# Kernel tuning notes

Hardware: AMD Instinct MI355X
Metric: run time of the kernel (lower is better)

Reference implementation:

```python
import jax, jax.numpy as jnp
import numpy as np
import math

LAMBDA_ATTRACT = 2.5
REPEL_STRENGTH = 0.15
EPSILON = 0.1  # repulsion distance offset
NORM_EPS = 1e-8
TAU_WEIGHT = 0.3
N = 8192


def _pairwise_angular(theta):
    # angular_distance(theta_i, theta_j) = min(|a-b|, 2*pi - |a-b|), shape [n, n]
    diff = jnp.abs(theta[:, None] - theta[None, :])
    return jnp.minimum(diff, 2.0 * math.pi - diff)


def setup_inputs() -> dict:
    key = jax.random.key(0)
    k1, k2 = jax.random.split(key)
    theta = jax.random.uniform(k1, (N,), dtype=jnp.float32, minval=-math.pi, maxval=math.pi)
    tau = jax.random.normal(k2, (N,), dtype=jnp.float32)
    return {"theta": theta, "tau": tau}


def reference(theta, tau):
    n = theta.shape[0]
    eye = jnp.eye(n, dtype=bool)

    d_theta = _pairwise_angular(theta)                      # [n, n]
    d_tau = jnp.abs(tau[:, None] - tau[None, :])            # [n, n]
    dist = d_theta + TAU_WEIGHT * d_tau

    # attention: exp(-lambda * dist), diagonal excluded, row-normalized
    dist_no_self = jnp.where(eye, jnp.inf, dist)
    scores = jnp.exp(-LAMBDA_ATTRACT * dist_no_self)
    attn = scores / jnp.sum(scores, axis=1, keepdims=True)

    cos_part = jnp.cos(theta)
    sin_part = jnp.sin(theta)
    R_x = attn @ cos_part
    R_y = attn @ sin_part

    # vectorized O(n^2) repulsion (replaces the python double loop)
    d = d_theta + EPSILON
    strength = REPEL_STRENGTH / (d * d)                     # [n, n]
    dx = cos_part[:, None] - cos_part[None, :]
    dy = sin_part[:, None] - sin_part[None, :]
    norm = jnp.sqrt(dx * dx + dy * dy) + NORM_EPS
    inv = jnp.where(eye, 0.0, strength / norm)              # mask i == j
    repel_force_x = jnp.sum(inv * dx, axis=1)
    repel_force_y = jnp.sum(inv * dy, axis=1)

    force_x = R_x + repel_force_x
    force_y = R_y + repel_force_y
    theta_out = jnp.arctan2(force_y, force_x)
    tau_out = attn @ tau
    return (theta_out, tau_out, attn)
```

## Files before the change

kernel.cpp:

```cpp
#include <hip/hip_runtime.h>
#include <math.h>

#define N_PTS 8192
#define TPB 256
#define RPB 8

#define C_LAMBDA   2.5f
#define C_REPEL    0.15f
#define C_EPS      0.1f
#define C_NORM_EPS 1e-8f
#define C_TAUW     0.3f
#define C_TWO_PI   6.28318530717958647692f
#define C_NEG_L_LOG2E (-3.60673760222240625f)

typedef float vf4 __attribute__((ext_vector_type(4)));

__device__ __forceinline__ float fast_exp2(float x) {
#if __has_builtin(__builtin_amdgcn_exp2f)
    return __builtin_amdgcn_exp2f(x);
#else
    return exp2f(x);
#endif
}
__device__ __forceinline__ float fast_sqrt(float x) {
#if __has_builtin(__builtin_amdgcn_sqrtf)
    return __builtin_amdgcn_sqrtf(x);
#else
    return sqrtf(x);
#endif
}
__device__ __forceinline__ float fast_rcp(float x) {
#if __has_builtin(__builtin_amdgcn_rcpf)
    return __builtin_amdgcn_rcpf(x);
#else
    return __fdividef(1.0f, x);
#endif
}
__device__ __forceinline__ float fast_log2(float x) {
#if __has_builtin(__builtin_amdgcn_logf)
    return __builtin_amdgcn_logf(x);
#else
    return log2f(x);
#endif
}

__device__ __forceinline__ float wave_reduce_sum(float v) {
    #pragma unroll
    for (int off = 32; off > 0; off >>= 1)
        v += __shfl_down(v, off, 64);
    return v;
}

__global__ void pack_kernel(const float* __restrict__ theta,
                            const float* __restrict__ tau,
                            float4* __restrict__ pk,
                            float2* __restrict__ pk2) {
    int i = blockIdx.x * blockDim.x + threadIdx.x;
    float t = theta[i];
    float u = tau[i];
    pk[i]  = make_float4(t, u, cosf(t), sinf(t));
    pk2[i] = make_float2(t, u);
}

__global__ __launch_bounds__(TPB) void phase1_kernel(
    const float4* __restrict__ pk,
    float* __restrict__ out,
    float* __restrict__ invsum)
{
    const int tid  = threadIdx.x;
    const int row0 = blockIdx.x * RPB;

    float th_i[RPB], ta_i[RPB], c_i[RPB], s_i[RPB];
    #pragma unroll
    for (int r = 0; r < RPB; ++r) {
        float4 p = pk[row0 + r];
        th_i[r] = p.x; ta_i[r] = p.y; c_i[r] = p.z; s_i[r] = p.w;
    }

    float a_sum[RPB], a_x[RPB], a_y[RPB], a_t[RPB], rp_x[RPB], rp_y[RPB];
    #pragma unroll
    for (int r = 0; r < RPB; ++r) {
        a_sum[r] = 0.f; a_x[r] = 0.f; a_y[r] = 0.f;
        a_t[r] = 0.f; rp_x[r] = 0.f; rp_y[r] = 0.f;
    }

    float4 cur = pk[tid];
    #pragma unroll 2
    for (int k = 0; k < N_PTS / TPB; ++k) {
        float4 nxt = pk[(tid + (k + 1) * TPB) & (N_PTS - 1)];
        #pragma unroll
        for (int r = 0; r < RPB; ++r) {
            float ad    = fabsf(th_i[r] - cur.x);
            float dth   = fminf(ad, C_TWO_PI - ad);
            float t     = fmaf(fabsf(ta_i[r] - cur.y), C_TAUW, dth);
            float score = fast_exp2(t * C_NEG_L_LOG2E);
            a_sum[r] += score;
            a_x[r]   = fmaf(score, cur.z, a_x[r]);
            a_y[r]   = fmaf(score, cur.w, a_y[r]);
            a_t[r]   = fmaf(score, cur.y, a_t[r]);

            float d   = dth + C_EPS;
            float dx  = c_i[r] - cur.z;
            float dy  = s_i[r] - cur.w;
            float q   = fmaf(dx, dx, dy * dy);
            float nrm = fast_sqrt(q) + C_NORM_EPS;
            float inv = fast_rcp(d * d * nrm);
            rp_x[r] = fmaf(inv, dx, rp_x[r]);
            rp_y[r] = fmaf(inv, dy, rp_y[r]);
        }
        cur = nxt;
    }

    __shared__ float red[RPB][6][TPB / 64];
    const int wave = tid >> 6;
    const int lane = tid & 63;
    #pragma unroll
    for (int r = 0; r < RPB; ++r) {
        float v0 = wave_reduce_sum(a_sum[r]);
        float v1 = wave_reduce_sum(a_x[r]);
        float v2 = wave_reduce_sum(a_y[r]);
        float v3 = wave_reduce_sum(a_t[r]);
        float v4 = wave_reduce_sum(rp_x[r]);
        float v5 = wave_reduce_sum(rp_y[r]);
        if (lane == 0) {
            red[r][0][wave] = v0; red[r][1][wave] = v1; red[r][2][wave] = v2;
            red[r][3][wave] = v3; red[r][4][wave] = v4; red[r][5][wave] = v5;
        }
    }
    __syncthreads();

    if (tid < RPB) {
        const int r = tid;
        float s = 0.f, x = 0.f, y = 0.f, t = 0.f, rx = 0.f, ry = 0.f;
        #pragma unroll
        for (int w = 0; w < TPB / 64; ++w) {
            s  += red[r][0][w]; x  += red[r][1][w]; y  += red[r][2][w];
            t  += red[r][3][w]; rx += red[r][4][w]; ry += red[r][5][w];
        }
        float4 p = pk[row0 + r];
        s -= 1.0f;
        x -= p.z;
        y -= p.w;
        t -= p.y;
        float invr = 1.0f / s;
        float fx = fmaf(x, invr, C_REPEL * rx);
        float fy = fmaf(y, invr, C_REPEL * ry);
        out[row0 + r]         = atan2f(fy, fx);
        out[N_PTS + row0 + r] = t * invr;
        invsum[row0 + r]      = invr;
    }
}

__global__ __launch_bounds__(TPB) void phase2_kernel(
    const float2* __restrict__ pk2,
    const float* __restrict__ invsum,
    float* __restrict__ attn)
{
    const int i   = blockIdx.x;
    const int tid = threadIdx.x;
    float2 pi   = pk2[i];
    float th_i  = pi.x;
    float ta_i  = pi.y;
    float l2inv = fast_log2(invsum[i]);
    float* __restrict__ row = attn + (size_t)i * N_PTS;
    const float4* __restrict__ pq = (const float4*)pk2;

    #pragma unroll
    for (int k = 0; k < N_PTS / (TPB * 4); ++k) {
        const int base = tid + k * TPB;
        float4 f1 = pq[2 * base];
        float4 f2 = pq[2 * base + 1];
        const int j0 = 4 * base;

        float ad0  = fabsf(th_i - f1.x);
        float dth0 = fminf(ad0, C_TWO_PI - ad0);
        float t0   = fmaf(fabsf(ta_i - f1.y), C_TAUW, dth0);
        float v0   = fast_exp2(fmaf(t0, C_NEG_L_LOG2E, l2inv));

        float ad1  = fabsf(th_i - f1.z);
        float dth1 = fminf(ad1, C_TWO_PI - ad1);
        float t1   = fmaf(fabsf(ta_i - f1.w), C_TAUW, dth1);
        float v1   = fast_exp2(fmaf(t1, C_NEG_L_LOG2E, l2inv));

        float ad2  = fabsf(th_i - f2.x);
        float dth2 = fminf(ad2, C_TWO_PI - ad2);
        float t2   = fmaf(fabsf(ta_i - f2.y), C_TAUW, dth2);
        float v2   = fast_exp2(fmaf(t2, C_NEG_L_LOG2E, l2inv));

        float ad3  = fabsf(th_i - f2.z);
        float dth3 = fminf(ad3, C_TWO_PI - ad3);
        float t3   = fmaf(fabsf(ta_i - f2.w), C_TAUW, dth3);
        float v3   = fast_exp2(fmaf(t3, C_NEG_L_LOG2E, l2inv));

        vf4 o = {v0, v1, v2, v3};
        __builtin_nontemporal_store(o, (vf4*)(row + j0));
    }

    __syncthreads();
    if (tid == 0) row[i] = 0.0f;
}

extern "C" void kernel_launch(void* const* d_in, const int* in_sizes, int n_in,
                              void* d_out, int out_size, void* d_ws, size_t ws_size,
                              hipStream_t stream) {
    const float* theta = (const float*)d_in[0];
    const float* tau   = (const float*)d_in[1];

    float4* pk     = (float4*)d_ws;
    float2* pk2    = (float2*)((char*)d_ws + 128 * 1024);
    float*  invsum = (float*)((char*)d_ws + 192 * 1024);
    float*  out    = (float*)d_out;
    float*  attn   = out + 2 * N_PTS;

    pack_kernel<<<N_PTS / 256, 256, 0, stream>>>(theta, tau, pk, pk2);
    phase1_kernel<<<N_PTS / RPB, TPB, 0, stream>>>(pk, out, invsum);
    phase2_kernel<<<N_PTS, TPB, 0, stream>>>(pk2, invsum, attn);
}
```

Baseline: 318.3 us.

## Fuse reduction and attention-write kernels into one per-row-block kernel

Merges the phase1 reduction kernel and the phase2 attention-matrix writer into a single kernel. Each block computes its row sums, shares the log2 inverse sums through LDS, then writes those rows of the attention matrix. This removes a launch and the invsum round trip, and lets the long write phase of some blocks overlap with the compute phase of others. RPB drops from 8 to 4 to give more blocks, and the nontemporal stores become plain stores, which may change cache behaviour on the 256MB output write.

Result: faster. 280.1 us (-12.0%).

```diff
diff --git a/kernel.cpp b/kernel.cpp
--- a/kernel.cpp
+++ b/kernel.cpp
@@ -3,7 +3,7 @@
 
 #define N_PTS 8192
 #define TPB 256
-#define RPB 8
+#define RPB 4
 
 #define C_LAMBDA   2.5f
 #define C_REPEL    0.15f
@@ -62,10 +62,10 @@
     pk2[i] = make_float2(t, u);
 }
 
-__global__ __launch_bounds__(TPB) void phase1_kernel(
+__global__ __launch_bounds__(TPB) void fused_kernel(
     const float4* __restrict__ pk,
-    float* __restrict__ out,
-    float* __restrict__ invsum)
+    const float4* __restrict__ pq,
+    float* __restrict__ out)
 {
     const int tid  = threadIdx.x;
     const int row0 = blockIdx.x * RPB;
@@ -112,6 +112,7 @@
     }
 
     __shared__ float red[RPB][6][TPB / 64];
+    __shared__ float l2s[RPB];
     const int wave = tid >> 6;
     const int lane = tid & 63;
     #pragma unroll
@@ -147,57 +148,54 @@
         float fy = fmaf(y, invr, C_REPEL * ry);
         out[row0 + r]         = atan2f(fy, fx);
         out[N_PTS + row0 + r] = t * invr;
-        invsum[row0 + r]      = invr;
-    }
-}
-
-__global__ __launch_bounds__(TPB) void phase2_kernel(
-    const float2* __restrict__ pk2,
-    const float* __restrict__ invsum,
-    float* __restrict__ attn)
-{
-    const int i   = blockIdx.x;
-    const int tid = threadIdx.x;
-    float2 pi   = pk2[i];
-    float th_i  = pi.x;
-    float ta_i  = pi.y;
-    float l2inv = fast_log2(invsum[i]);
-    float* __restrict__ row = attn + (size_t)i * N_PTS;
-    const float4* __restrict__ pq = (const float4*)pk2;
-
-    #pragma unroll
+        l2s[r] = fast_log2(invr);
+    }
+    __syncthreads();
+
+    float l2r[RPB];
+    #pragma unroll
+    for (int r = 0; r < RPB; ++r) l2r[r] = l2s[r];
+
+    float* __restrict__ attn = out + 2 * N_PTS;
+
+    #pragma unroll 2
     for (int k = 0; k < N_PTS / (TPB * 4); ++k) {
         const int base = tid + k * TPB;
         float4 f1 = pq[2 * base];
         float4 f2 = pq[2 * base + 1];
         const int j0 = 4 * base;
-
-        float ad0  = fabsf(th_i - f1.x);
-        float dth0 = fminf(ad0, C_TWO_PI - ad0);
-        float t0   = fmaf(fabsf(ta_i - f1.y), C_TAUW, dth0);
-        float v0   = fast_exp2(fmaf(t0, C_NEG_L_LOG2E, l2inv));
-
-        float ad1  = fabsf(th_i - f1.z);
-        float dth1 = fminf(ad1, C_TWO_PI - ad1);
-        float t1   = fmaf(fabsf(ta_i - f1.w), C_TAUW, dth1);
-        float v1   = fast_exp2(fmaf(t1, C_NEG_L_LOG2E, l2inv));
-
-        float ad2  = fabsf(th_i - f2.x);
-        float dth2 = fminf(ad2, C_TWO_PI - ad2);
-        float t2   = fmaf(fabsf(ta_i - f2.y), C_TAUW, dth2);
-        float v2   = fast_exp2(fmaf(t2, C_NEG_L_LOG2E, l2inv));
-
-        float ad3  = fabsf(th_i - f2.z);
-        float dth3 = fminf(ad3, C_TWO_PI - ad3);
-        float t3   = fmaf(fabsf(ta_i - f2.w), C_TAUW, dth3);
-        float v3   = fast_exp2(fmaf(t3, C_NEG_L_LOG2E, l2inv));
-
-        vf4 o = {v0, v1, v2, v3};
-        __builtin_nontemporal_store(o, (vf4*)(row + j0));
+        #pragma unroll
+        for (int r = 0; r < RPB; ++r) {
+            float ad0  = fabsf(th_i[r] - f1.x);
+            float dth0 = fminf(ad0, C_TWO_PI - ad0);
+            float t0   = fmaf(fabsf(ta_i[r] - f1.y), C_TAUW, dth0);
+            float v0   = fast_exp2(fmaf(t0, C_NEG_L_LOG2E, l2r[r]));
+
+            float ad1  = fabsf(th_i[r] - f1.z);
+            float dth1 = fminf(ad1, C_TWO_PI - ad1);
+            float t1   = fmaf(fabsf(ta_i[r] - f1.w), C_TAUW, dth1);
+            float v1   = fast_exp2(fmaf(t1, C_NEG_L_LOG2E, l2r[r]));
+
+            float ad2  = fabsf(th_i[r] - f2.x);
+            float dth2 = fminf(ad2, C_TWO_PI - ad2);
+            float t2   = fmaf(fabsf(ta_i[r] - f2.y), C_TAUW, dth2);
+            float v2   = fast_exp2(fmaf(t2, C_NEG_L_LOG2E, l2r[r]));
+
+            float ad3  = fabsf(th_i[r] - f2.z);
+            float dth3 = fminf(ad3, C_TWO_PI - ad3);
+            float t3   = fmaf(fabsf(ta_i[r] - f2.w), C_TAUW, dth3);
+            float v3   = fast_exp2(fmaf(t3, C_NEG_L_LOG2E, l2r[r]));
+
+            vf4 o = {v0, v1, v2, v3};
+            *(vf4*)(attn + (size_t)(row0 + r) * N_PTS + j0) = o;
+        }
     }
 
     __syncthreads();
-    if (tid == 0) row[i] = 0.0f;
+    if (tid < RPB) {
+        const int i = row0 + tid;
+        attn[(size_t)i * N_PTS + i] = 0.0f;
+    }
 }
 
 extern "C" void kernel_launch(void* const* d_in, const int* in_sizes, int n_in,
@@ -206,13 +204,10 @@
     const float* theta = (const float*)d_in[0];
     const float* tau   = (const float*)d_in[1];
 
-    float4* pk     = (float4*)d_ws;
-    float2* pk2    = (float2*)((char*)d_ws + 128 * 1024);
-    float*  invsum = (float*)((char*)d_ws + 192 * 1024);
-    float*  out    = (float*)d_out;
-    float*  attn   = out + 2 * N_PTS;
+    float4* pk  = (float4*)d_ws;
+    float2* pk2 = (float2*)((char*)d_ws + 128 * 1024);
+    float*  out = (float*)d_out;
 
     pack_kernel<<<N_PTS / 256, 256, 0, stream>>>(theta, tau, pk, pk2);
-    phase1_kernel<<<N_PTS / RPB, TPB, 0, stream>>>(pk, out, invsum);
-    phase2_kernel<<<N_PTS, TPB, 0, stream>>>(pk2, invsum, attn);
-}
+    fused_kernel<<<N_PTS / RPB, TPB, 0, stream>>>(pk, (const float4*)pk2, out);
+}
```
